# Optimization experiments

Measured on AMD Instinct MI355X. Metric: run time of the kernel, lower is better.

The kernel has to match this reference:

```python
import jax, jax.numpy as jnp
import numpy as np

B, C_IN, C_OUT, H, W, N = 2, 64, 64, 128, 128, 8
FACT = 4
H_SE = C_OUT // FACT               # 16 : SE bottleneck per direction
HID_ATTN = (N * C_OUT) // FACT     # 128: SortAttn hidden
G_ATTN = N * 2                     # 16 : SortAttn groups (group=2)
DIRECTIONS = [(1, 1), (1, -1), (-1, 1), (-1, -1), (1, 0), (-1, 0), (0, 1), (0, -1)]


def gconv1x1(x, w, groups):
    # x: [B,Cin,H,W], w: [Cout, Cin//groups] (1x1 grouped conv, no bias)
    b, cin, h, w_ = x.shape
    cout = w.shape[0]
    xg = x.reshape(b, groups, cin // groups, h * w_)
    wg = w.reshape(groups, cout // groups, cin // groups)
    y = jnp.einsum('bgip,goi->bgop', xg, wg)
    return y.reshape(b, cout, h, w_)


def channel_shuffle(x, g):
    b, c, h, w = x.shape
    return x.reshape(b, g, c // g, h, w).transpose(0, 2, 1, 3, 4).reshape(b, c, h, w)


def se2d(x, en_w, s_w, e_w, gate):
    # SE2d / SEGate2d with 1x1 en conv, n=N parallel attention branches
    y = jnp.einsum('bchw,oc->bohw', x, en_w)                      # en conv
    pooled = jnp.concatenate([y.mean((2, 3), keepdims=True),
                              y.max((2, 3), keepdims=True)], axis=1)  # [B,2C,1,1]
    hdn = jax.nn.relu(jnp.einsum('bchw,oc->bohw', pooled, s_w))   # [B,H_SE*N,1,1]
    attn = jax.nn.sigmoid(gconv1x1(hdn, e_w, N))                  # [B,N*C,1,1]
    b = y.shape[0]
    outs = y[:, None] * attn.reshape(b, N, C_OUT, 1, 1)           # [B,N,C,H,W]
    return jax.nn.sigmoid(outs) if gate else outs


def gru_dir(z, hh, h0c, d1, d2):
    # z, hh: [B,C,H,W]; h0c: [C]. Faithful to GRUDirection2d with |d| in {0,1}.
    flip_axes = tuple(ax for ax, dd in ((2, d1), (3, d2)) if dd < 0)
    if flip_axes:
        z = jnp.flip(z, flip_axes)
        hh = jnp.flip(hh, flip_axes)
    b, c, hgt, wid = z.shape
    if d1 != 0 and d2 != 0:
        # diagonal recurrence: h[i,j] = z*_h + (1-z)*h[i-1,j-1], border = h0
        init = jnp.broadcast_to(h0c[None, :, None], (b, c, wid))
        h0col = init[..., :1]

        def step(prev, zh):
            zt, ht = zh
            prev_s = jnp.concatenate([h0col, prev[..., :-1]], axis=-1)
            new = zt * ht + (1 - zt) * prev_s
            return new, new

        zm = jnp.moveaxis(z, 2, 0)
        hm = jnp.moveaxis(hh, 2, 0)
        _, out = jax.lax.scan(step, init, (zm, hm))
        out = jnp.moveaxis(out, 0, 2)
    else:
        axis = 2 if d1 != 0 else 3
        zm = jnp.moveaxis(z, axis, 0)
        hm = jnp.moveaxis(hh, axis, 0)
        init = jnp.broadcast_to(h0c[None, :, None], zm.shape[1:])

        def step(hprev, zh):
            zt, ht = zh
            new = zt * ht + (1 - zt) * hprev
            return new, new

        _, out = jax.lax.scan(step, init, (zm, hm))
        out = jnp.moveaxis(out, 0, axis)
    if flip_axes:
        out = jnp.flip(out, flip_axes)
    return out


def setup_inputs():
    key = jax.random.key(0)
    ks = jax.random.split(key, 13)
    s = 0.05
    return {
        'x': jax.random.normal(ks[0], (B, C_IN, H, W), jnp.float32),
        'h0': jax.random.normal(ks[1], (N, C_OUT), jnp.float32) * 0.1,
        'h_en_w': jax.random.normal(ks[2], (C_OUT, C_IN), jnp.float32) * s,
        'h_s_w': jax.random.normal(ks[3], (H_SE * N, 2 * C_OUT), jnp.float32) * s,
        'h_e_w': jax.random.normal(ks[4], (C_OUT * N, H_SE), jnp.float32) * s,
        'z_en_w': jax.random.normal(ks[5], (C_OUT, C_IN), jnp.float32) * s,
        'z_s_w': jax.random.normal(ks[6], (H_SE * N, 2 * C_OUT), jnp.float32) * s,
        'z_e_w': jax.random.normal(ks[7], (C_OUT * N, H_SE), jnp.float32) * s,
        'a_w1': jax.random.normal(ks[8], (HID_ATTN, (2 * N * C_OUT) // (2 * G_ATTN)), jnp.float32) * s,
        'a_w2': jax.random.normal(ks[9], (HID_ATTN, HID_ATTN // G_ATTN), jnp.float32) * s,
        'a_w3': jax.random.normal(ks[10], (HID_ATTN, HID_ATTN // G_ATTN), jnp.float32) * s,
        'a_w4': jax.random.normal(ks[11], (N * C_OUT, HID_ATTN // G_ATTN), jnp.float32) * s,
    }


def reference(x, h0, h_en_w, h_s_w, h_e_w, z_en_w, z_s_w, z_e_w, a_w1, a_w2, a_w3, a_w4):
    hhs = se2d(x, h_en_w, h_s_w, h_e_w, gate=False)   # candidate states, [B,N,C,H,W]
    zs = se2d(x, z_en_w, z_s_w, z_e_w, gate=True)     # update gates, [B,N,C,H,W]
    hs = [gru_dir(zs[:, i], hhs[:, i], h0[i], d1, d2)
          for i, (d1, d2) in enumerate(DIRECTIONS)]
    xcat = jnp.concatenate(hs, axis=1)                # [B, N*C, H, W]
    sorted_x = jnp.sort(xcat, axis=1)
    t = jnp.concatenate([xcat, sorted_x], axis=1)     # [B, 2*N*C, H, W]
    t = gconv1x1(t, a_w1, 2 * G_ATTN)
    t = channel_shuffle(t, G_ATTN)
    t = gconv1x1(t, a_w2, G_ATTN)
    t = channel_shuffle(t, G_ATTN)
    t = jax.nn.relu(gconv1x1(t, a_w3, G_ATTN))
    t = channel_shuffle(t, G_ATTN)
    scores = jax.nn.sigmoid(gconv1x1(t, a_w4, G_ATTN))
    b = xcat.shape[0]
    y = (xcat * scores).reshape(b, N, C_OUT, H, W).sum(axis=1)
    return y
```

## Files before the change

### kernel.cpp

```cpp
#include <hip/hip_runtime.h>
#include <cstdint>
#include <cstddef>

typedef unsigned int uint;
typedef unsigned short ushort;

#define DEVFN __device__ __forceinline__

DEVFN float bf2f(uint h) { return __uint_as_float(h << 16); }
DEVFN ushort f2bf(float x) {
  uint u = __float_as_uint(x);
  u = (u + 0x7FFFu + ((u >> 16) & 1u)) >> 16;
  return (ushort)u;
}
DEVFN uint encf(float x) {
  uint u = __float_as_uint(x);
  return (u & 0x80000000u) ? ~u : (u | 0x80000000u);
}
DEVFN float decf(uint e) {
  uint u = (e & 0x80000000u) ? (e ^ 0x80000000u) : ~e;
  return __uint_as_float(u);
}
DEVFN float sigmoidf(float x) { return 1.0f / (1.0f + __expf(-x)); }

__global__ void k_init(float* __restrict__ sums, uint* __restrict__ maxs) {
  int t = threadIdx.x;
  if (t < 256) sums[t] = 0.0f;
  else maxs[t - 256] = 0u;
}

__global__ __launch_bounds__(256) void k_conv(const float* __restrict__ x,
                                              const float* __restrict__ wh,
                                              const float* __restrict__ wz,
                                              uint* __restrict__ ypack) {
  __shared__ __align__(16) float xt[64][66];
  __shared__ __align__(16) float wls[2][64][64];
  const int tid = threadIdx.x;
  const int b = blockIdx.x >> 8;
  const int tile = blockIdx.x & 255;
  const int pix0 = tile * 64;

  for (int idx = tid; idx < 4096; idx += 256) {
    int o = idx >> 6, c = idx & 63;
    wls[0][c][o] = wh[idx];
    wls[1][c][o] = wz[idx];
  }
  const float* xb = x + ((size_t)b << 20);
  for (int idx = tid; idx < 4096; idx += 256) {
    int c = idx >> 6, p = idx & 63;
    xt[c][p] = xb[c * 16384 + pix0 + p];
  }
  __syncthreads();

  const int p = tid & 63, og = tid >> 6, o0 = og * 16;
  float fh[16], fz[16];
#pragma unroll
  for (int j = 0; j < 16; ++j) { fh[j] = 0.0f; fz[j] = 0.0f; }

  for (int c = 0; c < 64; ++c) {
    float xv = xt[c][p];
    const float4* whp = (const float4*)&wls[0][c][o0];
    const float4* wzp = (const float4*)&wls[1][c][o0];
#pragma unroll
    for (int jj = 0; jj < 4; ++jj) {
      float4 a = whp[jj], bb = wzp[jj];
      fh[jj * 4 + 0] += xv * a.x; fh[jj * 4 + 1] += xv * a.y;
      fh[jj * 4 + 2] += xv * a.z; fh[jj * 4 + 3] += xv * a.w;
      fz[jj * 4 + 0] += xv * bb.x; fz[jj * 4 + 1] += xv * bb.y;
      fz[jj * 4 + 2] += xv * bb.z; fz[jj * 4 + 3] += xv * bb.w;
    }
  }
  uint* orow = ypack + ((size_t)(b * 16384 + pix0 + p)) * 64 + o0;
#pragma unroll
  for (int jj = 0; jj < 4; ++jj) {
    uint4 pk;
    pk.x = (uint)f2bf(fh[jj * 4 + 0]) | ((uint)f2bf(fz[jj * 4 + 0]) << 16);
    pk.y = (uint)f2bf(fh[jj * 4 + 1]) | ((uint)f2bf(fz[jj * 4 + 1]) << 16);
    pk.z = (uint)f2bf(fh[jj * 4 + 2]) | ((uint)f2bf(fz[jj * 4 + 2]) << 16);
    pk.w = (uint)f2bf(fh[jj * 4 + 3]) | ((uint)f2bf(fz[jj * 4 + 3]) << 16);
    ((uint4*)orow)[jj] = pk;
  }
}

__global__ __launch_bounds__(256) void k_stats(const uint* __restrict__ ypack,
                                               float* __restrict__ sums,
                                               uint* __restrict__ maxs) {
  const int tid = threadIdx.x;
  const int b = blockIdx.x >> 6, slice = blockIdx.x & 63;
  const int c = tid & 63, pg = tid >> 6;
  float sh = 0.0f, sz = 0.0f, mh = -1e30f, mz = -1e30f;
  const uint* yb = ypack + ((size_t)(b * 16384 + slice * 256 + pg * 64)) * 64 + c;
  for (int ii = 0; ii < 64; ++ii) {
    uint u = yb[(size_t)ii * 64];
    float yh = bf2f(u & 0xffffu), yz = bf2f(u >> 16);
    sh += yh; sz += yz;
    mh = fmaxf(mh, yh); mz = fmaxf(mz, yz);
  }
  __shared__ float red[4][4][64];
  red[pg][0][c] = sh; red[pg][1][c] = sz; red[pg][2][c] = mh; red[pg][3][c] = mz;
  __syncthreads();
  const int stat = tid >> 6;
  float v0 = red[0][stat][c], v1 = red[1][stat][c];
  float v2 = red[2][stat][c], v3 = red[3][stat][c];
  if (stat < 2) {
    atomicAdd(&sums[(b * 2 + stat) * 64 + c], (v0 + v1) + (v2 + v3));
  } else {
    atomicMax(&maxs[(b * 2 + (stat - 2)) * 64 + c], encf(fmaxf(fmaxf(v0, v1), fmaxf(v2, v3))));
  }
}

__global__ void k_attn(const float* __restrict__ sums, const uint* __restrict__ maxs,
                       const float* __restrict__ hsw, const float* __restrict__ zsw,
                       const float* __restrict__ hew, const float* __restrict__ zew,
                       float* __restrict__ attnb) {
  __shared__ float pooled[2][2][128];
  __shared__ float hdn[2][2][128];
  const int tid = threadIdx.x;
  for (int idx = tid; idx < 512; idx += 256) {
    int hz = idx >> 8, bb = (idx >> 7) & 1, cc = idx & 127;
    float val;
    if (cc < 64) val = sums[(bb * 2 + hz) * 64 + cc] * (1.0f / 16384.0f);
    else val = decf(maxs[(bb * 2 + hz) * 64 + (cc - 64)]);
    pooled[hz][bb][cc] = val;
  }
  __syncthreads();
  for (int idx = tid; idx < 512; idx += 256) {
    int hz = idx >> 8, bb = (idx >> 7) & 1, o = idx & 127;
    const float* sw = hz ? zsw : hsw;
    float acc = 0.0f;
    for (int cc = 0; cc < 128; ++cc) acc += pooled[hz][bb][cc] * sw[o * 128 + cc];
    hdn[hz][bb][o] = fmaxf(acc, 0.0f);
  }
  __syncthreads();
  for (int idx = tid; idx < 2048; idx += 256) {
    int hz = idx >> 10, bb = (idx >> 9) & 1, o2 = idx & 511;
    const float* ew = hz ? zew : hew;
    const int gb = (o2 >> 6) * 16;
    float acc = 0.0f;
#pragma unroll
    for (int vv = 0; vv < 16; ++vv) acc += hdn[hz][bb][gb + vv] * ew[o2 * 16 + vv];
    attnb[(hz * 2 + bb) * 512 + o2] = sigmoidf(acc);
  }
}

__global__ __launch_bounds__(256) void k_scan(const uint* __restrict__ ypack,
                                              const float* __restrict__ attnb,
                                              const float* __restrict__ h0,
                                              ushort* __restrict__ xcat) {
  const int wid = blockIdx.x * 4 + (threadIdx.x >> 6);
  const int lane = threadIdx.x & 63;
  int i, b, s;
  if (wid < 2040) {
    i = wid / 510;
    int r = wid - i * 510;
    b = (r >= 255) ? 1 : 0;
    s = r - b * 255;
  } else {
    int w2 = wid - 2040;
    i = 4 + (w2 >> 8);
    int r = w2 & 255;
    b = r >> 7;
    s = r & 127;
  }
  int h0s, w0s, dh, dw, L;
  switch (i) {
    case 0: dh = 1;  dw = 1;
      if (s < 128) { h0s = s; w0s = 0; L = 128 - s; } else { h0s = 0; w0s = s - 127; L = 255 - s; }
      break;
    case 1: dh = 1;  dw = -1;
      if (s < 128) { h0s = 0; w0s = s; L = s + 1; } else { h0s = s - 127; w0s = 127; L = 255 - s; }
      break;
    case 2: dh = -1; dw = 1;
      if (s < 128) { h0s = s; w0s = 0; L = s + 1; } else { h0s = 127; w0s = s - 127; L = 255 - s; }
      break;
    case 3: dh = -1; dw = -1;
      if (s < 128) { h0s = 127; w0s = s; L = s + 1; } else { h0s = s - 128; w0s = 127; L = s - 127; }
      break;
    case 4: dh = 1;  dw = 0;  h0s = 0;   w0s = s; L = 128; break;
    case 5: dh = -1; dw = 0;  h0s = 127; w0s = s; L = 128; break;
    case 6: dh = 0;  dw = 1;  h0s = s;   w0s = 0; L = 128; break;
    default: dh = 0; dw = -1; h0s = s;   w0s = 127; L = 128; break;
  }
  const float ah = attnb[b * 512 + i * 64 + lane];
  const float az = attnb[1024 + b * 512 + i * 64 + lane];
  float hp = h0[i * 64 + lane];

  const int pos = b * 16384 + h0s * 128 + w0s;
  const int dstep = dh * 128 + dw;
  const uint* yp = ypack + (size_t)pos * 64 + lane;
  ushort* xp = xcat + (size_t)pos * 512 + i * 64 + lane;
  const ptrdiff_t ystep = (ptrdiff_t)dstep * 64;
  const ptrdiff_t xstep = (ptrdiff_t)dstep * 512;

#pragma unroll 4
  for (int t = 0; t < L; ++t) {
    uint u = *yp;
    float yh = bf2f(u & 0xffffu), yz = bf2f(u >> 16);
    float zt = sigmoidf(yz * az);
    hp = hp + zt * (yh * ah - hp);
    *xp = f2bf(hp);
    yp += ystep;
    xp += xstep;
  }
}

__global__ __launch_bounds__(256, 2) void k_final(const ushort* __restrict__ xcat,
                                                  const float* __restrict__ a_w1,
                                                  const float* __restrict__ a_w2,
                                                  const float* __restrict__ a_w3,
                                                  const float* __restrict__ a_w4,
                                                  float* __restrict__ out) {
  __shared__ __align__(16) float w1s[128 * 32];
  __shared__ float tb1[4][128];
  __shared__ float tb2[4][128];
  __shared__ __align__(16) float otile[64][68];

  const int tid = threadIdx.x;
  const int lane = tid & 63;
  const int wslot = tid >> 6;
  const int b = blockIdx.x >> 8;
  const int tile = blockIdx.x & 255;
  const int pix0 = tile * 64;

  for (int idx = tid; idx < 4096; idx += 256) {
    int o = idx >> 5, ci = idx & 31;
    w1s[o * 32 + ((ci + (o >> 2)) & 31)] = a_w1[idx];
  }

  float w2a[8], w2b[8], w3a[8], w3b[8], w4r[64];
  {
    const float4* p;
    p = (const float4*)(a_w2 + lane * 8);        ((float4*)w2a)[0] = p[0]; ((float4*)w2a)[1] = p[1];
    p = (const float4*)(a_w2 + 512 + lane * 8);  ((float4*)w2b)[0] = p[0]; ((float4*)w2b)[1] = p[1];
    p = (const float4*)(a_w3 + lane * 8);        ((float4*)w3a)[0] = p[0]; ((float4*)w3a)[1] = p[1];
    p = (const float4*)(a_w3 + 512 + lane * 8);  ((float4*)w3b)[0] = p[0]; ((float4*)w3b)[1] = p[1];
    p = (const float4*)(a_w4 + lane * 64);
#pragma unroll
    for (int n = 0; n < 16; ++n) ((float4*)w4r)[n] = p[n];
  }
  __syncthreads();

  const int q = lane >> 2, m4 = lane & 3;
  const int base1 = 64 * ((lane >> 3) & 1) + (lane >> 4);
  const int base3 = 64 * ((lane >> 2) & 1) + (lane >> 3);

  for (int it = 0; it < 16; ++it) {
    const int px = wslot * 16 + it;
    const int pix = pix0 + px;

    float v[8], s[8];
    {
      const uint4 pk = *(const uint4*)(xcat + (((size_t)(b * 16384 + pix)) << 9) + lane * 8);
      v[0] = bf2f(pk.x & 0xffffu); v[1] = bf2f(pk.x >> 16);
      v[2] = bf2f(pk.y & 0xffffu); v[3] = bf2f(pk.y >> 16);
      v[4] = bf2f(pk.z & 0xffffu); v[5] = bf2f(pk.z >> 16);
      v[6] = bf2f(pk.w & 0xffffu); v[7] = bf2f(pk.w >> 16);
    }
#pragma unroll
    for (int r = 0; r < 8; ++r) s[r] = v[r];

#pragma unroll
    for (int k = 2; k <= 512; k <<= 1) {
#pragma unroll
      for (int j = k >> 1; j >= 1; j >>= 1) {
        if (j >= 8) {
          const int m = j >> 3;
          const bool upper = (lane & m) != 0;
          const bool asc = (lane & (k >> 3)) == 0;
          const bool takeMin = (upper != asc);
#pragma unroll
          for (int r = 0; r < 8; ++r) {
            float o = __shfl_xor(s[r], m, 64);
            float mn = fminf(s[r], o), mx = fmaxf(s[r], o);
            s[r] = takeMin ? mn : mx;
          }
        } else if (k < 8) {
#pragma unroll
          for (int r = 0; r < 8; ++r) {
            if ((r & j) == 0) {
              int r2 = r | j;
              float mn = fminf(s[r], s[r2]), mx = fmaxf(s[r], s[r2]);
              if ((r & k) == 0) { s[r] = mn; s[r2] = mx; }
              else { s[r] = mx; s[r2] = mn; }
            }
          }
        } else {
          const bool asc = (lane & (k >> 3)) == 0;
#pragma unroll
          for (int r = 0; r < 8; ++r) {
            if ((r & j) == 0) {
              int r2 = r | j;
              float mn = fminf(s[r], s[r2]), mx = fmaxf(s[r], s[r2]);
              s[r] = asc ? mn : mx;
              s[r2] = asc ? mx : mn;
            }
          }
        }
      }
    }

    float pa[4], pb[4];
#pragma unroll
    for (int u = 0; u < 4; ++u) {
      const float* wV = &w1s[(4 * q + u) * 32];
      const float* wS = &w1s[(64 + 4 * q + u) * 32];
      float aV = 0.0f, aS = 0.0f;
#pragma unroll
      for (int r = 0; r < 8; ++r) {
        const int ci = m4 * 8 + r;
        aV += v[r] * wV[(ci + q) & 31];
        aS += s[r] * wS[(ci + q + 16) & 31];
      }
      pa[u] = aV; pb[u] = aS;
    }
#pragma unroll
    for (int u = 0; u < 4; ++u) {
      pa[u] += __shfl_xor(pa[u], 1, 64);
      pa[u] += __shfl_xor(pa[u], 2, 64);
      pb[u] += __shfl_xor(pb[u], 1, 64);
      pb[u] += __shfl_xor(pb[u], 2, 64);
    }
    const float t1a = (m4 == 0) ? pa[0] : (m4 == 1) ? pa[1] : (m4 == 2) ? pa[2] : pa[3];
    const float t1b = (m4 == 0) ? pb[0] : (m4 == 1) ? pb[1] : (m4 == 2) ? pb[2] : pb[3];

    tb1[wslot][lane] = t1a;
    tb1[wslot][64 + lane] = t1b;
    __syncthreads();

    float a2 = 0.0f, b2 = 0.0f;
#pragma unroll
    for (int kk = 0; kk < 8; ++kk) {
      a2 += tb1[wslot][base1 + 8 * kk] * w2a[kk];
      b2 += tb1[wslot][base1 + 8 * kk + 4] * w2b[kk];
    }
    tb2[wslot][lane] = a2;
    tb2[wslot][64 + lane] = b2;
    __syncthreads();

    float a3 = 0.0f, b3 = 0.0f;
#pragma unroll
    for (int kk = 0; kk < 8; ++kk) {
      a3 += tb2[wslot][base1 + 8 * kk] * w3a[kk];
      b3 += tb2[wslot][base1 + 8 * kk + 4] * w3b[kk];
    }
    tb1[wslot][lane] = fmaxf(a3, 0.0f);
    tb1[wslot][64 + lane] = fmaxf(b3, 0.0f);
    __syncthreads();

    float in4[8];
#pragma unroll
    for (int kk = 0; kk < 8; ++kk) in4[kk] = tb1[wslot][base3 + 8 * kk];

    float prod[8];
#pragma unroll
    for (int rr = 0; rr < 8; ++rr) {
      float acc = 0.0f;
#pragma unroll
      for (int kk = 0; kk < 8; ++kk) acc += in4[kk] * w4r[rr * 8 + kk];
      prod[rr] = v[rr] * sigmoidf(acc);
    }
#pragma unroll
    for (int rr = 0; rr < 8; ++rr) {
      prod[rr] += __shfl_xor(prod[rr], 8, 64);
      prod[rr] += __shfl_xor(prod[rr], 16, 64);
      prod[rr] += __shfl_xor(prod[rr], 32, 64);
    }
    if (lane < 8) {
      float4* dst = (float4*)&otile[px][lane * 8];
      dst[0] = make_float4(prod[0], prod[1], prod[2], prod[3]);
      dst[1] = make_float4(prod[4], prod[5], prod[6], prod[7]);
    }
  }
  __syncthreads();

  for (int c = wslot; c < 64; c += 4) {
    out[(((size_t)(b * 64 + c)) << 14) + pix0 + lane] = otile[lane][c];
  }
}

extern "C" void kernel_launch(void* const* d_in, const int* in_sizes, int n_in,
                              void* d_out, int out_size, void* d_ws, size_t ws_size,
                              hipStream_t stream) {
  const float* x      = (const float*)d_in[0];
  const float* h0     = (const float*)d_in[1];
  const float* h_en_w = (const float*)d_in[2];
  const float* h_s_w  = (const float*)d_in[3];
  const float* h_e_w  = (const float*)d_in[4];
  const float* z_en_w = (const float*)d_in[5];
  const float* z_s_w  = (const float*)d_in[6];
  const float* z_e_w  = (const float*)d_in[7];
  const float* a_w1   = (const float*)d_in[8];
  const float* a_w2   = (const float*)d_in[9];
  const float* a_w3   = (const float*)d_in[10];
  const float* a_w4   = (const float*)d_in[11];
  float* out = (float*)d_out;

  char* ws = (char*)d_ws;
  uint*   ypack = (uint*)ws;
  ushort* xcat  = (ushort*)(ws + ((size_t)8 << 20));
  float*  sums  = (float*)(ws + ((size_t)40 << 20));
  uint*   maxs  = (uint*)(ws + ((size_t)40 << 20) + 1024);
  float*  attnb = (float*)(ws + ((size_t)40 << 20) + 4096);

  hipLaunchKernelGGL(k_init, dim3(1), dim3(512), 0, stream, sums, maxs);
  hipLaunchKernelGGL(k_conv, dim3(512), dim3(256), 0, stream, x, h_en_w, z_en_w, ypack);
  hipLaunchKernelGGL(k_stats, dim3(128), dim3(256), 0, stream, ypack, sums, maxs);
  hipLaunchKernelGGL(k_attn, dim3(1), dim3(256), 0, stream, sums, maxs, h_s_w, z_s_w,
                     h_e_w, z_e_w, attnb);
  hipLaunchKernelGGL(k_scan, dim3(766), dim3(256), 0, stream, ypack, attnb, h0, xcat);
  hipLaunchKernelGGL(k_final, dim3(512), dim3(256), 0, stream, xcat, a_w1, a_w2, a_w3,
                     a_w4, out);
}
```

Baseline: 274.6 us.

## Split stats/attn/final kernels finer, prefetch scan loads, move w4 to LDS

k_stats and k_attn now launch more blocks, so the reductions and the small attention MLP run in parallel instead of on a few blocks. k_scan loads the next four recurrence inputs ahead of the dependent update chain, and uses fma for the update. k_final moves its 64-entry per-lane w4 register array into LDS as packed bf16 and raises launch bounds to 4 blocks per SM. It also shrinks the pixel tile to 16 and drops block-wide barriers that only guarded per-wave buffers. The trade-offs are a lossier w4 weight, less coalesced output stores from the smaller tile, and more redundant weight staging across blocks.

```diff
diff --git a/kernel.cpp b/kernel.cpp
--- a/kernel.cpp
+++ b/kernel.cpp
@@ -86,11 +86,11 @@
                                                float* __restrict__ sums,
                                                uint* __restrict__ maxs) {
   const int tid = threadIdx.x;
-  const int b = blockIdx.x >> 6, slice = blockIdx.x & 63;
+  const int b = blockIdx.x >> 8, slice = blockIdx.x & 255;
   const int c = tid & 63, pg = tid >> 6;
   float sh = 0.0f, sz = 0.0f, mh = -1e30f, mz = -1e30f;
-  const uint* yb = ypack + ((size_t)(b * 16384 + slice * 256 + pg * 64)) * 64 + c;
-  for (int ii = 0; ii < 64; ++ii) {
+  const uint* yb = ypack + ((size_t)(b * 16384 + slice * 64 + pg * 16)) * 64 + c;
+  for (int ii = 0; ii < 16; ++ii) {
     uint u = yb[(size_t)ii * 64];
     float yh = bf2f(u & 0xffffu), yz = bf2f(u >> 16);
     sh += yh; sz += yz;
@@ -113,32 +113,30 @@
                        const float* __restrict__ hsw, const float* __restrict__ zsw,
                        const float* __restrict__ hew, const float* __restrict__ zew,
                        float* __restrict__ attnb) {
-  __shared__ float pooled[2][2][128];
-  __shared__ float hdn[2][2][128];
+  __shared__ float pooled[128];
+  __shared__ float hdn[128];
   const int tid = threadIdx.x;
-  for (int idx = tid; idx < 512; idx += 256) {
-    int hz = idx >> 8, bb = (idx >> 7) & 1, cc = idx & 127;
+  const int hz = blockIdx.x >> 1, bb = blockIdx.x & 1;
+  if (tid < 128) {
     float val;
-    if (cc < 64) val = sums[(bb * 2 + hz) * 64 + cc] * (1.0f / 16384.0f);
-    else val = decf(maxs[(bb * 2 + hz) * 64 + (cc - 64)]);
-    pooled[hz][bb][cc] = val;
-  }
-  __syncthreads();
-  for (int idx = tid; idx < 512; idx += 256) {
-    int hz = idx >> 8, bb = (idx >> 7) & 1, o = idx & 127;
+    if (tid < 64) val = sums[(bb * 2 + hz) * 64 + tid] * (1.0f / 16384.0f);
+    else val = decf(maxs[(bb * 2 + hz) * 64 + (tid - 64)]);
+    pooled[tid] = val;
+  }
+  __syncthreads();
+  if (tid < 128) {
     const float* sw = hz ? zsw : hsw;
     float acc = 0.0f;
-    for (int cc = 0; cc < 128; ++cc) acc += pooled[hz][bb][cc] * sw[o * 128 + cc];
-    hdn[hz][bb][o] = fmaxf(acc, 0.0f);
-  }
-  __syncthreads();
-  for (int idx = tid; idx < 2048; idx += 256) {
-    int hz = idx >> 10, bb = (idx >> 9) & 1, o2 = idx & 511;
-    const float* ew = hz ? zew : hew;
+    for (int cc = 0; cc < 128; ++cc) acc += pooled[cc] * sw[tid * 128 + cc];
+    hdn[tid] = fmaxf(acc, 0.0f);
+  }
+  __syncthreads();
+  const float* ew = hz ? zew : hew;
+  for (int o2 = tid; o2 < 512; o2 += 256) {
     const int gb = (o2 >> 6) * 16;
     float acc = 0.0f;
 #pragma unroll
-    for (int vv = 0; vv < 16; ++vv) acc += hdn[hz][bb][gb + vv] * ew[o2 * 16 + vv];
+    for (int vv = 0; vv < 16; ++vv) acc += hdn[gb + vv] * ew[o2 * 16 + vv];
     attnb[(hz * 2 + bb) * 512 + o2] = sigmoidf(acc);
   }
 }
@@ -192,51 +190,71 @@
   const ptrdiff_t ystep = (ptrdiff_t)dstep * 64;
   const ptrdiff_t xstep = (ptrdiff_t)dstep * 512;
 
-#pragma unroll 4
-  for (int t = 0; t < L; ++t) {
-    uint u = *yp;
-    float yh = bf2f(u & 0xffffu), yz = bf2f(u >> 16);
-    float zt = sigmoidf(yz * az);
-    hp = hp + zt * (yh * ah - hp);
-    *xp = f2bf(hp);
-    yp += ystep;
-    xp += xstep;
-  }
-}
-
-__global__ __launch_bounds__(256, 2) void k_final(const ushort* __restrict__ xcat,
+#define PROC1(u) { float yh = bf2f((u) & 0xffffu), yz = bf2f((u) >> 16); \
+                   float zt = sigmoidf(yz * az);                          \
+                   hp = fmaf(zt, fmaf(yh, ah, -hp), hp);                  \
+                   *xp = f2bf(hp); xp += xstep; }
+
+  uint c0 = 0, c1 = 0, c2 = 0, c3 = 0;
+  c0 = yp[0];
+  if (1 < L) c1 = yp[ystep];
+  if (2 < L) c2 = yp[2 * ystep];
+  if (3 < L) c3 = yp[3 * ystep];
+
+  for (int base = 0; base < L; base += 4) {
+    uint b0 = c0, b1 = c1, b2 = c2, b3 = c3;
+    const uint* ypn = yp + (ptrdiff_t)(base + 4) * ystep;
+    if (base + 4 < L) {
+      c0 = ypn[0];
+      if (base + 5 < L) c1 = ypn[ystep];
+      if (base + 6 < L) c2 = ypn[2 * ystep];
+      if (base + 7 < L) c3 = ypn[3 * ystep];
+    }
+    PROC1(b0);
+    if (base + 1 < L) PROC1(b1);
+    if (base + 2 < L) PROC1(b2);
+    if (base + 3 < L) PROC1(b3);
+  }
+#undef PROC1
+}
+
+__global__ __launch_bounds__(256, 4) void k_final(const ushort* __restrict__ xcat,
                                                   const float* __restrict__ a_w1,
                                                   const float* __restrict__ a_w2,
                                                   const float* __restrict__ a_w3,
                                                   const float* __restrict__ a_w4,
                                                   float* __restrict__ out) {
   __shared__ __align__(16) float w1s[128 * 32];
+  __shared__ uint w4p[32 * 64];
   __shared__ float tb1[4][128];
   __shared__ float tb2[4][128];
-  __shared__ __align__(16) float otile[64][68];
+  __shared__ __align__(16) float otile[16][68];
 
   const int tid = threadIdx.x;
   const int lane = tid & 63;
   const int wslot = tid >> 6;
-  const int b = blockIdx.x >> 8;
-  const int tile = blockIdx.x & 255;
-  const int pix0 = tile * 64;
+  const int b = blockIdx.x >> 10;
+  const int tile = blockIdx.x & 1023;
+  const int pix0 = tile * 16;
 
   for (int idx = tid; idx < 4096; idx += 256) {
     int o = idx >> 5, ci = idx & 31;
     w1s[o * 32 + ((ci + (o >> 2)) & 31)] = a_w1[idx];
   }
-
-  float w2a[8], w2b[8], w3a[8], w3b[8], w4r[64];
+  for (int idx = tid; idx < 2048; idx += 256) {
+    int rk2 = idx >> 6, l = idx & 63;
+    int rr = rk2 >> 2, kp = rk2 & 3;
+    const float* src = a_w4 + ((l * 8 + rr) * 8 + 2 * kp);
+    w4p[rk2 * 64 + l] = (uint)f2bf(src[0]) | ((uint)f2bf(src[1]) << 16);
+  }
+
+  float w2a[8], w2b[8], w3a[8], w3b[8];
   {
     const float4* p;
     p = (const float4*)(a_w2 + lane * 8);        ((float4*)w2a)[0] = p[0]; ((float4*)w2a)[1] = p[1];
     p = (const float4*)(a_w2 + 512 + lane * 8);  ((float4*)w2b)[0] = p[0]; ((float4*)w2b)[1] = p[1];
     p = (const float4*)(a_w3 + lane * 8);        ((float4*)w3a)[0] = p[0]; ((float4*)w3a)[1] = p[1];
     p = (const float4*)(a_w3 + 512 + lane * 8);  ((float4*)w3b)[0] = p[0]; ((float4*)w3b)[1] = p[1];
-    p = (const float4*)(a_w4 + lane * 64);
-#pragma unroll
-    for (int n = 0; n < 16; ++n) ((float4*)w4r)[n] = p[n];
   }
   __syncthreads();
 
@@ -244,8 +262,8 @@
   const int base1 = 64 * ((lane >> 3) & 1) + (lane >> 4);
   const int base3 = 64 * ((lane >> 2) & 1) + (lane >> 3);
 
-  for (int it = 0; it < 16; ++it) {
-    const int px = wslot * 16 + it;
+  for (int it = 0; it < 4; ++it) {
+    const int px = wslot * 4 + it;
     const int pix = pix0 + px;
 
     float v[8], s[8];
@@ -325,7 +343,6 @@
 
     tb1[wslot][lane] = t1a;
     tb1[wslot][64 + lane] = t1b;
-    __syncthreads();
 
     float a2 = 0.0f, b2 = 0.0f;
 #pragma unroll
@@ -335,7 +352,6 @@
     }
     tb2[wslot][lane] = a2;
     tb2[wslot][64 + lane] = b2;
-    __syncthreads();
 
     float a3 = 0.0f, b3 = 0.0f;
 #pragma unroll
@@ -345,7 +361,6 @@
     }
     tb1[wslot][lane] = fmaxf(a3, 0.0f);
     tb1[wslot][64 + lane] = fmaxf(b3, 0.0f);
-    __syncthreads();
 
     float in4[8];
 #pragma unroll
@@ -356,7 +371,12 @@
     for (int rr = 0; rr < 8; ++rr) {
       float acc = 0.0f;
 #pragma unroll
-      for (int kk = 0; kk < 8; ++kk) acc += in4[kk] * w4r[rr * 8 + kk];
+      for (int kp = 0; kp < 4; ++kp) {
+        uint pw = w4p[(rr * 4 + kp) * 64 + lane];
+        float wlo = __uint_as_float(pw << 16);
+        float whi = __uint_as_float(pw & 0xffff0000u);
+        acc += in4[2 * kp] * wlo + in4[2 * kp + 1] * whi;
+      }
       prod[rr] = v[rr] * sigmoidf(acc);
     }
 #pragma unroll
@@ -373,8 +393,9 @@
   }
   __syncthreads();
 
-  for (int c = wslot; c < 64; c += 4) {
-    out[(((size_t)(b * 64 + c)) << 14) + pix0 + lane] = otile[lane][c];
+  for (int idx = tid; idx < 1024; idx += 256) {
+    int px = idx & 15, c = idx >> 4;
+    out[(((size_t)(b * 64 + c)) << 14) + pix0 + px] = otile[px][c];
   }
 }
 
@@ -404,10 +425,10 @@
 
   hipLaunchKernelGGL(k_init, dim3(1), dim3(512), 0, stream, sums, maxs);
   hipLaunchKernelGGL(k_conv, dim3(512), dim3(256), 0, stream, x, h_en_w, z_en_w, ypack);
-  hipLaunchKernelGGL(k_stats, dim3(128), dim3(256), 0, stream, ypack, sums, maxs);
-  hipLaunchKernelGGL(k_attn, dim3(1), dim3(256), 0, stream, sums, maxs, h_s_w, z_s_w,
+  hipLaunchKernelGGL(k_stats, dim3(512), dim3(256), 0, stream, ypack, sums, maxs);
+  hipLaunchKernelGGL(k_attn, dim3(4), dim3(256), 0, stream, sums, maxs, h_s_w, z_s_w,
                      h_e_w, z_e_w, attnb);
   hipLaunchKernelGGL(k_scan, dim3(766), dim3(256), 0, stream, ypack, attnb, h0, xcat);
-  hipLaunchKernelGGL(k_final, dim3(512), dim3(256), 0, stream, xcat, a_w1, a_w2, a_w3,
+  hipLaunchKernelGGL(k_final, dim3(2048), dim3(256), 0, stream, xcat, a_w1, a_w2, a_w3,
                      a_w4, out);
 }
```

Measured after the change: 306.5 us. 1.12x slower.
